# Performance work log

Measured on AMD Instinct MI355X. Metric: run time of the kernel, lower is better.

The kernel has to match this reference:

```python
import jax, jax.numpy as jnp
import numpy as np

C = 1024          # embed_dim
H = 16            # num_heads
D = C // H        # head_dim = 64
M = 64            # memory_size
HID = 4 * C       # mlp hidden
EPS = 1e-5


def _ln(x, g, b):
    mu = jnp.mean(x, axis=-1, keepdims=True)
    var = jnp.mean(jnp.square(x - mu), axis=-1, keepdims=True)
    return (x - mu) * jax.lax.rsqrt(var + EPS) * g + b


def setup_inputs() -> dict:
    key = jax.random.key(0)
    ks = jax.random.split(key, 16)
    s = 0.02
    return {
        'x': jax.random.normal(ks[0], (2, 2048, C), jnp.float32),
        'memory': jax.random.normal(ks[1], (1, M, C), jnp.float32),
        'ln1_g': jnp.ones((C,), jnp.float32),
        'ln1_b': jnp.zeros((C,), jnp.float32),
        'w_qkv': jax.random.normal(ks[2], (C, 3 * C), jnp.float32) * s,
        'b_qkv': jnp.zeros((3 * C,), jnp.float32),
        'w_out': jax.random.normal(ks[3], (C, C), jnp.float32) * s,
        'b_out': jnp.zeros((C,), jnp.float32),
        'w_mem': jax.random.normal(ks[4], (C, C), jnp.float32) * s,
        'b_mem': jnp.zeros((C,), jnp.float32),
        'ln2_g': jnp.ones((C,), jnp.float32),
        'ln2_b': jnp.zeros((C,), jnp.float32),
        'w_fc1': jax.random.normal(ks[5], (C, HID), jnp.float32) * s,
        'b_fc1': jnp.zeros((HID,), jnp.float32),
        'w_fc2': jax.random.normal(ks[6], (HID, C), jnp.float32) * s,
        'b_fc2': jnp.zeros((C,), jnp.float32),
    }


def reference(x, memory, ln1_g, ln1_b, w_qkv, b_qkv, w_out, b_out,
              w_mem, b_mem, ln2_g, ln2_b, w_fc1, b_fc1, w_fc2, b_fc2):
    B, T, _ = x.shape
    scale = 1.0 / np.sqrt(D)

    # --- InfiniAttention on norm1(x) ---
    h = _ln(x, ln1_g, ln1_b)
    qkv = (h @ w_qkv + b_qkv).reshape(B, T, 3, H, D)
    q = qkv[:, :, 0].transpose(0, 2, 1, 3)  # (B,H,T,D)
    k = qkv[:, :, 1].transpose(0, 2, 1, 3)
    v = qkv[:, :, 2].transpose(0, 2, 1, 3)

    # local full softmax attention over the window of T tokens
    attn = jax.nn.softmax(jnp.einsum('bhtd,bhsd->bhts', q, k) * scale, axis=-1)
    local_out = jnp.einsum('bhts,bhsd->bhtd', attn, v)

    # compressive memory read: mem acts as both K and V
    mem = (memory @ w_mem + b_mem)                 # (1,M,C)
    mem_kv = jnp.broadcast_to(mem, (B, M, C)).reshape(B, M, H, D).transpose(0, 2, 1, 3)  # (B,H,M,D)
    mem_attn = jax.nn.softmax(jnp.einsum('bhtd,bhmd->bhtm', q, mem_kv) * scale, axis=-1)
    mem_out = jnp.einsum('bhtm,bhmd->bhtd', mem_attn, mem_kv)

    out = (local_out + mem_out).transpose(0, 2, 1, 3).reshape(B, T, C)
    out = out @ w_out + b_out
    x = x + out

    # --- MLP on norm2(x) ---
    h2 = _ln(x, ln2_g, ln2_b)
    h2 = jax.nn.gelu(h2 @ w_fc1 + b_fc1, approximate=False)
    x = x + h2 @ w_fc2 + b_fc2
    return x
```

## Files before the change

### kernel.cpp

```cpp
#include <hip/hip_runtime.h>
#include <hip/hip_bf16.h>

typedef unsigned short u16;
typedef unsigned int u32;
typedef short bf16x8 __attribute__((ext_vector_type(8)));
typedef float f32x4 __attribute__((ext_vector_type(4)));

__device__ __forceinline__ u16 f2bf(float x) {
    u32 u = __float_as_uint(x);
    u32 rounding = 0x7FFFu + ((u >> 16) & 1u);
    return (u16)((u + rounding) >> 16);
}

__device__ __forceinline__ void gload_lds16(const u16* g, u16* l) {
    __builtin_amdgcn_global_load_lds((const __attribute__((address_space(1))) void*)g,
                                     (__attribute__((address_space(3))) void*)l, 16, 0, 0);
}

__device__ __forceinline__ int xcd_swz(int id, int nwg) {
    int q = nwg >> 3, r = nwg & 7;
    int x = id & 7, k = id >> 3;
    return (x < r ? x * (q + 1) : r * (q + 1) + (x - r) * q) + k;
}

__global__ __launch_bounds__(256) void ln_kernel(const float* __restrict__ in,
                                                 const float* __restrict__ g,
                                                 const float* __restrict__ b,
                                                 u16* __restrict__ outp) {
    int tok = blockIdx.x;
    int t = threadIdx.x;
    const float4* row = (const float4*)(in + (size_t)tok * 1024);
    float4 v = row[t];
    float s = v.x + v.y + v.z + v.w;
    float sq = v.x * v.x + v.y * v.y + v.z * v.z + v.w * v.w;
#pragma unroll
    for (int off = 32; off >= 1; off >>= 1) {
        s += __shfl_xor(s, off);
        sq += __shfl_xor(sq, off);
    }
    __shared__ float rs[4], rq[4];
    int lane = t & 63, w = t >> 6;
    if (lane == 0) { rs[w] = s; rq[w] = sq; }
    __syncthreads();
    s = rs[0] + rs[1] + rs[2] + rs[3];
    sq = rq[0] + rq[1] + rq[2] + rq[3];
    float mean = s * (1.0f / 1024.0f);
    float var = sq * (1.0f / 1024.0f) - mean * mean;
    float rstd = rsqrtf(var + 1e-5f);
    float4 gg = ((const float4*)g)[t];
    float4 bb = ((const float4*)b)[t];
    u16* o = outp + (size_t)tok * 1024 + t * 4;
    o[0] = f2bf((v.x - mean) * rstd * gg.x + bb.x);
    o[1] = f2bf((v.y - mean) * rstd * gg.y + bb.y);
    o[2] = f2bf((v.z - mean) * rstd * gg.z + bb.z);
    o[3] = f2bf((v.w - mean) * rstd * gg.w + bb.w);
}

__global__ __launch_bounds__(256) void transpose_w(const float* __restrict__ W,
                                                   u16* __restrict__ WT, int K, int N) {
    __shared__ float tile[32][33];
    int n0 = blockIdx.x * 32, k0 = blockIdx.y * 32;
    int tx = threadIdx.x & 31, ty = threadIdx.x >> 5;
#pragma unroll
    for (int i = 0; i < 4; i++) {
        int kk = ty + i * 8;
        tile[kk][tx] = W[(size_t)(k0 + kk) * N + n0 + tx];
    }
    __syncthreads();
#pragma unroll
    for (int i = 0; i < 4; i++) {
        int nn = ty + i * 8;
        WT[(size_t)(n0 + nn) * K + k0 + tx] = f2bf(tile[tx][nn]);
    }
}

__global__ void convert_bf(const float* __restrict__ in, u16* __restrict__ outp, int n) {
    int i = blockIdx.x * blockDim.x + threadIdx.x;
    if (i < n) outp[i] = f2bf(in[i]);
}

__global__ __launch_bounds__(256) void prep_kv(const u16* __restrict__ src,
                                               u32* __restrict__ kdst, u32* __restrict__ vdst,
                                               long bstride, int rstride, int koff, int voff) {
    int t = blockIdx.x, bh = blockIdx.y;
    int b = bh >> 4, h = bh & 15;
    int tid = threadIdx.x;
    const u16* kS = src + (size_t)b * bstride + (size_t)(t * 64) * rstride + koff + h * 64;
    const u16* vS = src + (size_t)b * bstride + (size_t)(t * 64) * rstride + voff + h * 64;
    u32* kD = kdst + ((size_t)bh * gridDim.x + t) * 2048;
    u32* vD = vdst + ((size_t)bh * gridDim.x + t) * 2048;
#pragma unroll
    for (int c = 0; c < 2; c++) {
        int idx = tid + c * 256;
        int row = idx >> 3, blk = idx & 7;
        uint4 q = *(const uint4*)&kS[(size_t)row * rstride + blk * 8];
        *(uint4*)&kD[row * 32 + ((blk ^ (row & 7)) << 2)] = q;
    }
#pragma unroll
    for (int c = 0; c < 2; c++) {
        int idx = tid + c * 256;
        int drow = idx >> 3, kblk = idx & 7;
        u32 vv[4];
#pragma unroll
        for (int e = 0; e < 4; e++) {
            int j0 = kblk * 8 + 2 * e, j1 = j0 + 1;
            int kv0 = 16 * (j0 & 3) + (j0 >> 2);
            int kv1 = 16 * (j1 & 3) + (j1 >> 2);
            vv[e] = (u32)vS[(size_t)kv0 * rstride + drow] |
                    ((u32)vS[(size_t)kv1 * rstride + drow] << 16);
        }
        *(uint4*)&vD[drow * 32 + ((kblk ^ (drow & 7)) << 2)] = *(uint4*)vv;
    }
}

template <int MODE, int BM>
__global__ __launch_bounds__(256) void gemm_bf16(const u16* A, const u16* BT,
                                                 const float* __restrict__ bias,
                                                 const float* res, void* outv,
                                                 int M, int N, int K) {
    __shared__ __align__(16) u16 As[3][BM * 32];
    __shared__ __align__(16) u16 Bs[3][128 * 32];
    constexpr int MI = BM / 32;
    int gx = gridDim.x, gy = gridDim.y;
    int id = blockIdx.y * gx + blockIdx.x;
    int id2 = xcd_swz(id, gx * gy);
    int bx = id2 / gy, by = id2 % gy;
    int rowBase = by * BM, colBase = bx * 128;
    int t = threadIdx.x, lane = t & 63, w = t >> 6;
    int wr = w >> 1, wc = w & 1, r = lane & 15, g = lane >> 4;

    int lrow = lane >> 2;
    int scol = (lane & 3) * 8;
    const u16* b0 = BT + (size_t)(colBase + (w * 2 + 0) * 16 + lrow) * K + scol;
    const u16* b1 = BT + (size_t)(colBase + (w * 2 + 1) * 16 + lrow) * K + scol;
    int lB0 = (w * 2 + 0) * 512;
    int lB1 = (w * 2 + 1) * 512;
    const u16* a0;
    const u16* a1 = nullptr;
    int lA0, lA1 = 0;
    if constexpr (BM == 128) {
        a0 = A + (size_t)(rowBase + (w * 2 + 0) * 16 + lrow) * K + scol;
        a1 = A + (size_t)(rowBase + (w * 2 + 1) * 16 + lrow) * K + scol;
        lA0 = (w * 2 + 0) * 512;
        lA1 = (w * 2 + 1) * 512;
    } else {
        a0 = A + (size_t)(rowBase + w * 16 + lrow) * K + scol;
        lA0 = w * 512;
    }

    auto stage = [&](int k0, u16* Ab, u16* Bb) {
        gload_lds16(a0 + k0, Ab + lA0);
        if constexpr (BM == 128) gload_lds16(a1 + k0, Ab + lA1);
        gload_lds16(b0 + k0, Bb + lB0);
        gload_lds16(b1 + k0, Bb + lB1);
    };

    u16 *pA0 = &As[0][0], *pA1 = &As[1][0], *pA2 = &As[2][0];
    u16 *pB0 = &Bs[0][0], *pB1 = &Bs[1][0], *pB2 = &Bs[2][0];

    f32x4 acc[MI][4] = {};
    int nk = K >> 5;
    stage(0, pA0, pB0);
    stage(32, pA1, pB1);
    for (int kt = 0; kt < nk; kt++) {
        if (kt + 2 < nk) {
            stage((kt + 2) << 5, pA2, pB2);
            if constexpr (BM == 128) asm volatile("s_waitcnt vmcnt(8)" ::: "memory");
            else                     asm volatile("s_waitcnt vmcnt(6)" ::: "memory");
        } else if (kt + 1 < nk) {
            if constexpr (BM == 128) asm volatile("s_waitcnt vmcnt(4)" ::: "memory");
            else                     asm volatile("s_waitcnt vmcnt(3)" ::: "memory");
        } else {
            asm volatile("s_waitcnt vmcnt(0)" ::: "memory");
        }
        __builtin_amdgcn_s_barrier();
        bf16x8 af[MI], bfr[4];
#pragma unroll
        for (int mi = 0; mi < MI; mi++)
            af[mi] = *(const bf16x8*)&pA0[(wr * (BM / 2) + mi * 16 + r) * 32 + g * 8];
#pragma unroll
        for (int ni = 0; ni < 4; ni++)
            bfr[ni] = *(const bf16x8*)&pB0[(wc * 64 + ni * 16 + r) * 32 + g * 8];
        __builtin_amdgcn_s_setprio(1);
#pragma unroll
        for (int mi = 0; mi < MI; mi++)
#pragma unroll
            for (int ni = 0; ni < 4; ni++)
                acc[mi][ni] = __builtin_amdgcn_mfma_f32_16x16x32_bf16(af[mi], bfr[ni], acc[mi][ni], 0, 0, 0);
        __builtin_amdgcn_s_setprio(0);
        __builtin_amdgcn_s_barrier();
        u16* tA = pA0; pA0 = pA1; pA1 = pA2; pA2 = tA;
        u16* tB = pB0; pB0 = pB1; pB1 = pB2; pB2 = tB;
    }

#pragma unroll
    for (int mi = 0; mi < MI; mi++) {
#pragma unroll
        for (int ni = 0; ni < 4; ni++) {
#pragma unroll
            for (int rr = 0; rr < 4; rr++) {
                int grow = rowBase + wr * (BM / 2) + mi * 16 + g * 4 + rr;
                int gcol = colBase + wc * 64 + ni * 16 + r;
                if (grow < M) {
                    float v = acc[mi][ni][rr] + bias[gcol];
                    if constexpr (MODE == 1) {
                        v = 0.5f * v * (1.0f + erff(v * 0.70710678118f));
                    }
                    if constexpr (MODE == 2) {
                        ((float*)outv)[(size_t)grow * N + gcol] = v + res[(size_t)grow * N + gcol];
                    } else {
                        ((u16*)outv)[(size_t)grow * N + gcol] = f2bf(v);
                    }
                }
            }
        }
    }
}

__global__ __launch_bounds__(256) void attn_kernel(const u16* __restrict__ qkv,
                                                   const u32* __restrict__ ktiled,
                                                   const u32* __restrict__ vttiled,
                                                   const u32* __restrict__ memK,
                                                   const u32* __restrict__ memVT,
                                                   u16* __restrict__ outp) {
    __shared__ __align__(16) u32 KB[2][2048];
    __shared__ __align__(16) u32 VB[2][2048];
    __shared__ __align__(16) u32 P32[64][32];
    const int T = 2048, C3 = 3072;
    int id = blockIdx.y * 32 + blockIdx.x;
    int id2 = xcd_swz(id, 1024);
    int bh = id2 >> 5, qt = id2 & 31;
    int b = bh >> 4, h = bh & 15;
    int t0 = qt * 64;
    int tid = threadIdx.x, lane = tid & 63, w = tid >> 6, r = lane & 15, g = lane >> 4;
    int swz = r & 7;
    size_t qkvb = (size_t)b * T * C3;

    const u16* qrow = qkv + qkvb + (size_t)(t0 + w * 16 + r) * C3 + h * 64;
    bf16x8 aq0 = *(const bf16x8*)(qrow + g * 8);
    bf16x8 aq1 = *(const bf16x8*)(qrow + 32 + g * 8);
#pragma unroll
    for (int i = 0; i < 8; i++) {
        float f0 = __uint_as_float(((u32)(u16)aq0[i]) << 16) * 0.18033688f;
        float f1 = __uint_as_float(((u32)(u16)aq1[i]) << 16) * 0.18033688f;
        aq0[i] = (short)f2bf(f0);
        aq1[i] = (short)f2bf(f1);
    }

    f32x4 O[4] = {};
    float m_[4] = {-1e30f, -1e30f, -1e30f, -1e30f};
    float lv[4] = {0.f, 0.f, 0.f, 0.f};

    auto stage = [&](int t, int buf) {
        const u32 *kb, *vb;
        if (t < 32) {
            kb = ktiled + ((size_t)bh * 32 + t) * 2048;
            vb = vttiled + ((size_t)bh * 32 + t) * 2048;
        } else {
            kb = memK + (size_t)h * 2048;
            vb = memVT + (size_t)h * 2048;
        }
        gload_lds16((const u16*)(kb + tid * 4), (u16*)&KB[buf][tid * 4]);
        gload_lds16((const u16*)(kb + 1024 + tid * 4), (u16*)&KB[buf][1024 + tid * 4]);
        gload_lds16((const u16*)(vb + tid * 4), (u16*)&VB[buf][tid * 4]);
        gload_lds16((const u16*)(vb + 1024 + tid * 4), (u16*)&VB[buf][1024 + tid * 4]);
    };

    auto compute = [&](int buf) {
        f32x4 sv[4];
#pragma unroll
        for (int n = 0; n < 4; n++) {
            int row = n * 16 + r;
            bf16x8 bk0 = *(const bf16x8*)&KB[buf][row * 32 + ((g ^ swz) << 2)];
            bf16x8 bk1 = *(const bf16x8*)&KB[buf][row * 32 + (((4 + g) ^ swz) << 2)];
            f32x4 z = {0.f, 0.f, 0.f, 0.f};
            z = __builtin_amdgcn_mfma_f32_16x16x32_bf16(aq0, bk0, z, 0, 0, 0);
            z = __builtin_amdgcn_mfma_f32_16x16x32_bf16(aq1, bk1, z, 0, 0, 0);
            sv[n] = z;
        }
        float mxl[4];
#pragma unroll
        for (int rr = 0; rr < 4; rr++)
            mxl[rr] = fmaxf(fmaxf(sv[0][rr], sv[1][rr]), fmaxf(sv[2][rr], sv[3][rr]));
        float dmax = fmaxf(fmaxf(mxl[0] - m_[0], mxl[1] - m_[1]),
                           fmaxf(mxl[2] - m_[2], mxl[3] - m_[3]));
        if (!__all(dmax <= 8.0f)) {
#pragma unroll
            for (int rr = 0; rr < 4; rr++) {
                float mxr = mxl[rr];
#pragma unroll
                for (int off = 8; off >= 1; off >>= 1) mxr = fmaxf(mxr, __shfl_xor(mxr, off));
                float mn = fmaxf(m_[rr], mxr);
                float alpha = exp2f(m_[rr] - mn);
                m_[rr] = mn;
                lv[rr] *= alpha;
#pragma unroll
                for (int n = 0; n < 4; n++) O[n][rr] *= alpha;
            }
        }
#pragma unroll
        for (int rr = 0; rr < 4; rr++) {
            int q = w * 16 + g * 4 + rr;
            float p0 = exp2f(sv[0][rr] - m_[rr]);
            float p1 = exp2f(sv[1][rr] - m_[rr]);
            float p2 = exp2f(sv[2][rr] - m_[rr]);
            float p3 = exp2f(sv[3][rr] - m_[rr]);
            lv[rr] += (p0 + p1) + (p2 + p3);
            uint2 pw;
            pw.x = __builtin_amdgcn_perm(__float_as_uint(p1), __float_as_uint(p0), 0x07060302u);
            pw.y = __builtin_amdgcn_perm(__float_as_uint(p3), __float_as_uint(p2), 0x07060302u);
            *(uint2*)&P32[q][4 * ((r >> 1) ^ (q & 7)) + 2 * (r & 1)] = pw;
        }
        bf16x8 ap0 = *(const bf16x8*)&P32[w * 16 + r][(g ^ swz) << 2];
        bf16x8 ap1 = *(const bf16x8*)&P32[w * 16 + r][((4 + g) ^ swz) << 2];
#pragma unroll
        for (int n = 0; n < 4; n++) {
            int row = n * 16 + r;
            bf16x8 bv0 = *(const bf16x8*)&VB[buf][row * 32 + ((g ^ swz) << 2)];
            bf16x8 bv1 = *(const bf16x8*)&VB[buf][row * 32 + (((4 + g) ^ swz) << 2)];
            O[n] = __builtin_amdgcn_mfma_f32_16x16x32_bf16(ap0, bv0, O[n], 0, 0, 0);
            O[n] = __builtin_amdgcn_mfma_f32_16x16x32_bf16(ap1, bv1, O[n], 0, 0, 0);
        }
    };

    float outLocal[4][4];
    stage(0, 0);
    __syncthreads();
    for (int tt = 0; tt <= 32; tt++) {
        if (tt < 32) stage(tt + 1, (tt + 1) & 1);
        if (tt == 32) {
#pragma unroll
            for (int rr = 0; rr < 4; rr++) {
                float ls = lv[rr];
#pragma unroll
                for (int off = 8; off >= 1; off >>= 1) ls += __shfl_xor(ls, off);
                float inv = 1.0f / ls;
#pragma unroll
                for (int n = 0; n < 4; n++) outLocal[n][rr] = O[n][rr] * inv;
                m_[rr] = -1e30f;
                lv[rr] = 0.f;
            }
#pragma unroll
            for (int n = 0; n < 4; n++) { f32x4 z = {0.f, 0.f, 0.f, 0.f}; O[n] = z; }
        }
        compute(tt & 1);
        __syncthreads();
    }
#pragma unroll
    for (int rr = 0; rr < 4; rr++) {
        float ls = lv[rr];
#pragma unroll
        for (int off = 8; off >= 1; off >>= 1) ls += __shfl_xor(ls, off);
        float inv = 1.0f / ls;
        int row = t0 + w * 16 + g * 4 + rr;
#pragma unroll
        for (int n = 0; n < 4; n++) {
            float v2 = outLocal[n][rr] + O[n][rr] * inv;
            outp[((size_t)(b * T + row)) * 1024 + h * 64 + n * 16 + r] = f2bf(v2);
        }
    }
}

extern "C" void kernel_launch(void* const* d_in, const int* in_sizes, int n_in,
                              void* d_out, int out_size, void* d_ws, size_t ws_size,
                              hipStream_t stream) {
    const float* x      = (const float*)d_in[0];
    const float* memory = (const float*)d_in[1];
    const float* ln1_g  = (const float*)d_in[2];
    const float* ln1_b  = (const float*)d_in[3];
    const float* w_qkv  = (const float*)d_in[4];
    const float* b_qkv  = (const float*)d_in[5];
    const float* w_out  = (const float*)d_in[6];
    const float* b_out  = (const float*)d_in[7];
    const float* w_mem  = (const float*)d_in[8];
    const float* b_mem  = (const float*)d_in[9];
    const float* ln2_g  = (const float*)d_in[10];
    const float* ln2_b  = (const float*)d_in[11];
    const float* w_fc1  = (const float*)d_in[12];
    const float* b_fc1  = (const float*)d_in[13];
    const float* w_fc2  = (const float*)d_in[14];
    const float* b_fc2  = (const float*)d_in[15];
    float* out = (float*)d_out;

    char* ws = (char*)d_ws;
    size_t off = 0;
    auto alloc = [&](size_t bytes) { size_t o = off; off += (bytes + 255) & ~(size_t)255; return o; };
    u16* h_bf    = (u16*)(ws + alloc((size_t)4096 * 1024 * 2));
    u16* qkv_bf  = (u16*)(ws + alloc((size_t)4096 * 3072 * 2));
    u16* attn_bf = (u16*)(ws + alloc((size_t)4096 * 1024 * 2));
    u16* g1_bf   = (u16*)(ws + alloc((size_t)4096 * 4096 * 2));
    u16* mem_bf  = (u16*)(ws + alloc((size_t)64 * 1024 * 2));
    u16* memA_bf = (u16*)(ws + alloc((size_t)64 * 1024 * 2));
    u16* wqkvT   = (u16*)(ws + alloc((size_t)3072 * 1024 * 2));
    u16* woutT   = (u16*)(ws + alloc((size_t)1024 * 1024 * 2));
    u16* wmemT   = (u16*)(ws + alloc((size_t)1024 * 1024 * 2));
    u16* wfc1T   = (u16*)(ws + alloc((size_t)4096 * 1024 * 2));
    u16* wfc2T   = (u16*)(ws + alloc((size_t)1024 * 4096 * 2));

    u32* ktiled  = (u32*)g1_bf;
    u32* vttiled = ktiled + (size_t)1024 * 2048;
    u32* memK    = vttiled + (size_t)1024 * 2048;
    u32* memVT   = memK + (size_t)16 * 2048;

    transpose_w<<<dim3(3072 / 32, 1024 / 32), 256, 0, stream>>>(w_qkv, wqkvT, 1024, 3072);
    transpose_w<<<dim3(1024 / 32, 1024 / 32), 256, 0, stream>>>(w_out, woutT, 1024, 1024);
    transpose_w<<<dim3(1024 / 32, 1024 / 32), 256, 0, stream>>>(w_mem, wmemT, 1024, 1024);
    transpose_w<<<dim3(4096 / 32, 1024 / 32), 256, 0, stream>>>(w_fc1, wfc1T, 1024, 4096);
    transpose_w<<<dim3(1024 / 32, 4096 / 32), 256, 0, stream>>>(w_fc2, wfc2T, 4096, 1024);
    convert_bf<<<dim3(256), 256, 0, stream>>>(memory, memA_bf, 64 * 1024);

    ln_kernel<<<dim3(4096), 256, 0, stream>>>(x, ln1_g, ln1_b, h_bf);

    gemm_bf16<0, 128><<<dim3(24, 32), 256, 0, stream>>>(h_bf, wqkvT, b_qkv, nullptr, qkv_bf, 4096, 3072, 1024);

    gemm_bf16<0, 64><<<dim3(8, 1), 256, 0, stream>>>(memA_bf, wmemT, b_mem, nullptr, mem_bf, 64, 1024, 1024);

    prep_kv<<<dim3(32, 32), 256, 0, stream>>>(qkv_bf, ktiled, vttiled,
                                              (long)2048 * 3072, 3072, 1024, 2048);
    prep_kv<<<dim3(1, 16), 256, 0, stream>>>(mem_bf, memK, memVT, 0, 1024, 0, 0);

    attn_kernel<<<dim3(32, 32), 256, 0, stream>>>(qkv_bf, ktiled, vttiled, memK, memVT, attn_bf);

    gemm_bf16<2, 64><<<dim3(8, 64), 256, 0, stream>>>(attn_bf, woutT, b_out, x, out, 4096, 1024, 1024);

    ln_kernel<<<dim3(4096), 256, 0, stream>>>(out, ln2_g, ln2_b, h_bf);

    gemm_bf16<1, 128><<<dim3(32, 32), 256, 0, stream>>>(h_bf, wfc1T, b_fc1, nullptr, g1_bf, 4096, 4096, 1024);

    gemm_bf16<2, 64><<<dim3(8, 64), 256, 0, stream>>>(g1_bf, wfc2T, b_fc2, out, out, 4096, 1024, 4096);

    (void)in_sizes; (void)n_in; (void)out_size; (void)ws_size;
}
```

Measured before the change: 482.2 us.

## Add 256x256-tile 512-thread bf16 GEMM for QKV and FC1 projections

```diff
diff --git a/kernel.cpp b/kernel.cpp
--- a/kernel.cpp
+++ b/kernel.cpp
@@ -110,6 +110,140 @@
                     ((u32)vS[(size_t)kv1 * rstride + drow] << 16);
         }
         *(uint4*)&vD[drow * 32 + ((kblk ^ (drow & 7)) << 2)] = *(uint4*)vv;
+    }
+}
+
+template <int MODE>
+__global__ __launch_bounds__(512, 2) void gemm256(const u16* A, const u16* BT,
+                                                  const float* __restrict__ bias,
+                                                  void* outv, int M, int N, int K) {
+    __shared__ __align__(16) u16 lds[2][4][8192];
+    int gx = gridDim.x, gy = gridDim.y;
+    int id = blockIdx.y * gx + blockIdx.x;
+    int id2 = xcd_swz(id, gx * gy);
+    int bx = id2 / gy, by = id2 % gy;
+    int rowBase = by * 256, colBase = bx * 256;
+    int tid = threadIdx.x, lane = tid & 63, w = tid >> 6;
+    int wm = w >> 2, wn = w & 3, bh = wn >> 1;
+    int r = lane & 15, g = lane >> 4, rb = r & 7;
+
+    int srow = tid >> 3;
+    int swblk = (tid & 7) ^ (srow & 7);
+    const u16* aS0 = A + (size_t)(rowBase + srow) * K + swblk * 8;
+    const u16* aS1 = A + (size_t)(rowBase + 128 + srow) * K + swblk * 8;
+    const u16* bS0 = BT + (size_t)(colBase + srow) * K + swblk * 8;
+    const u16* bS1 = BT + (size_t)(colBase + 128 + srow) * K + swblk * 8;
+    size_t j64 = (size_t)64 * K;
+
+    auto stageH = [&](int bufi, int h, const u16* src, int kt) {
+        const u16* s = src + kt * 64;
+        u16* d = &lds[bufi][h][tid * 8];
+        gload_lds16(s, d);
+        gload_lds16(s + j64, d + 4096);
+    };
+
+    f32x4 acc[8][4] = {};
+    int NK = K >> 6;
+    stageH(0, 0, aS0, 0); stageH(0, 1, aS1, 0);
+    stageH(0, 2, bS0, 0); stageH(0, 3, bS1, 0);
+
+    for (int kt = 0; kt < NK; kt++) {
+        int cur = kt & 1, nxt = cur ^ 1;
+        bool hasNext = (kt + 1 < NK);
+        const u16* Ah = &lds[cur][wm][0];
+        const u16* Bh = &lds[cur][2 + bh][0];
+        int bro = (wn & 1) * 64;
+
+        if (hasNext) {
+            stageH(nxt, 0, aS0, kt + 1);
+            asm volatile("s_waitcnt vmcnt(2)" ::: "memory");
+        } else {
+            asm volatile("s_waitcnt vmcnt(0)" ::: "memory");
+        }
+        __builtin_amdgcn_s_barrier();
+
+        bf16x8 aL[4][2], bb[4][2];
+#pragma unroll
+        for (int mi = 0; mi < 4; mi++)
+#pragma unroll
+            for (int kk = 0; kk < 2; kk++)
+                aL[mi][kk] = *(const bf16x8*)&Ah[(mi * 16 + r) * 64 + ((kk * 4 + g) ^ rb) * 8];
+#pragma unroll
+        for (int ni = 0; ni < 2; ni++)
+#pragma unroll
+            for (int kk = 0; kk < 2; kk++)
+                bb[ni][kk] = *(const bf16x8*)&Bh[(bro + ni * 16 + r) * 64 + ((kk * 4 + g) ^ rb) * 8];
+        __builtin_amdgcn_s_setprio(1);
+#pragma unroll
+        for (int mi = 0; mi < 4; mi++)
+#pragma unroll
+            for (int ni = 0; ni < 2; ni++)
+#pragma unroll
+                for (int kk = 0; kk < 2; kk++)
+                    acc[mi][ni] = __builtin_amdgcn_mfma_f32_16x16x32_bf16(aL[mi][kk], bb[ni][kk], acc[mi][ni], 0, 0, 0);
+        __builtin_amdgcn_s_setprio(0);
+
+        if (hasNext) stageH(nxt, 1, aS1, kt + 1);
+#pragma unroll
+        for (int ni = 2; ni < 4; ni++)
+#pragma unroll
+            for (int kk = 0; kk < 2; kk++)
+                bb[ni][kk] = *(const bf16x8*)&Bh[(bro + ni * 16 + r) * 64 + ((kk * 4 + g) ^ rb) * 8];
+        __builtin_amdgcn_s_setprio(1);
+#pragma unroll
+        for (int mi = 0; mi < 4; mi++)
+#pragma unroll
+            for (int ni = 2; ni < 4; ni++)
+#pragma unroll
+                for (int kk = 0; kk < 2; kk++)
+                    acc[mi][ni] = __builtin_amdgcn_mfma_f32_16x16x32_bf16(aL[mi][kk], bb[ni][kk], acc[mi][ni], 0, 0, 0);
+        __builtin_amdgcn_s_setprio(0);
+
+        if (hasNext) stageH(nxt, 2, bS0, kt + 1);
+        bf16x8 aH[4][2];
+#pragma unroll
+        for (int mi = 0; mi < 4; mi++)
+#pragma unroll
+            for (int kk = 0; kk < 2; kk++)
+                aH[mi][kk] = *(const bf16x8*)&Ah[((mi + 4) * 16 + r) * 64 + ((kk * 4 + g) ^ rb) * 8];
+        __builtin_amdgcn_s_setprio(1);
+#pragma unroll
+        for (int mi = 0; mi < 4; mi++)
+#pragma unroll
+            for (int ni = 2; ni < 4; ni++)
+#pragma unroll
+                for (int kk = 0; kk < 2; kk++)
+                    acc[mi + 4][ni] = __builtin_amdgcn_mfma_f32_16x16x32_bf16(aH[mi][kk], bb[ni][kk], acc[mi + 4][ni], 0, 0, 0);
+        __builtin_amdgcn_s_setprio(0);
+
+        if (hasNext) stageH(nxt, 3, bS1, kt + 1);
+        __builtin_amdgcn_s_setprio(1);
+#pragma unroll
+        for (int mi = 0; mi < 4; mi++)
+#pragma unroll
+            for (int ni = 0; ni < 2; ni++)
+#pragma unroll
+                for (int kk = 0; kk < 2; kk++)
+                    acc[mi + 4][ni] = __builtin_amdgcn_mfma_f32_16x16x32_bf16(aH[mi][kk], bb[ni][kk], acc[mi + 4][ni], 0, 0, 0);
+        __builtin_amdgcn_s_setprio(0);
+        __builtin_amdgcn_s_barrier();
+    }
+
+#pragma unroll
+    for (int mi = 0; mi < 8; mi++) {
+#pragma unroll
+        for (int ni = 0; ni < 4; ni++) {
+#pragma unroll
+            for (int rr = 0; rr < 4; rr++) {
+                int grow = rowBase + wm * 128 + mi * 16 + g * 4 + rr;
+                int gcol = colBase + wn * 64 + ni * 16 + r;
+                float v = acc[mi][ni][rr] + bias[gcol];
+                if constexpr (MODE == 1) {
+                    v = 0.5f * v * (1.0f + erff(v * 0.70710678118f));
+                }
+                ((u16*)outv)[(size_t)grow * N + gcol] = f2bf(v);
+            }
+        }
     }
 }
 
@@ -411,7 +545,7 @@
 
     ln_kernel<<<dim3(4096), 256, 0, stream>>>(x, ln1_g, ln1_b, h_bf);
 
-    gemm_bf16<0, 128><<<dim3(24, 32), 256, 0, stream>>>(h_bf, wqkvT, b_qkv, nullptr, qkv_bf, 4096, 3072, 1024);
+    gemm256<0><<<dim3(12, 16), 512, 0, stream>>>(h_bf, wqkvT, b_qkv, qkv_bf, 4096, 3072, 1024);
 
     gemm_bf16<0, 64><<<dim3(8, 1), 256, 0, stream>>>(memA_bf, wmemT, b_mem, nullptr, mem_bf, 64, 1024, 1024);
 
@@ -425,7 +559,7 @@
 
     ln_kernel<<<dim3(4096), 256, 0, stream>>>(out, ln2_g, ln2_b, h_bf);
 
-    gemm_bf16<1, 128><<<dim3(32, 32), 256, 0, stream>>>(h_bf, wfc1T, b_fc1, nullptr, g1_bf, 4096, 4096, 1024);
+    gemm256<1><<<dim3(16, 16), 512, 0, stream>>>(h_bf, wfc1T, b_fc1, g1_bf, 4096, 4096, 1024);
 
     gemm_bf16<2, 64><<<dim3(8, 64), 256, 0, stream>>>(g1_bf, wfc2T, b_fc2, out, out, 4096, 1024, 4096);
 
```

Result: faster. 447.2 us (-7.2%).
